# Performance work log

Measured on AMD Instinct MI355X. Metric: run time of the kernel, lower is better.

## Reference

```python
import jax, jax.numpy as jnp
import numpy as np

TEMPERATURE = 0.1


def setup_inputs() -> dict:
    key = jax.random.key(0)
    ks = jax.random.split(key, 8)
    B = 16384
    yonehot = jax.random.uniform(ks[0], (B, 10), dtype=jnp.float32)
    # MLP params (10 -> 128 -> 512 -> 784); uniform-positive so proba > 0 strictly
    W1 = jax.random.uniform(ks[1], (10, 128), dtype=jnp.float32) * 0.05
    b1 = jax.random.uniform(ks[2], (128,), dtype=jnp.float32) * 0.01
    W2 = jax.random.uniform(ks[3], (128, 512), dtype=jnp.float32) * 0.05
    b2 = jax.random.uniform(ks[4], (512,), dtype=jnp.float32) * 0.01
    W3 = jax.random.uniform(ks[5], (512, 784), dtype=jnp.float32) * 0.05
    b3 = jax.random.uniform(ks[6], (784,), dtype=jnp.float32) * 0.01
    return {"yonehot": yonehot, "W1": W1, "b1": b1, "W2": W2, "b2": b2,
            "W3": W3, "b3": b3, "k": 128}


def _mlp(yonehot, W1, b1, W2, b2, W3, b3):
    h = jax.nn.relu(yonehot @ W1 + b1)
    h = jax.nn.relu(h @ W2 + b2)
    return jax.nn.relu(h @ W3 + b3)  # (B, 784) probability map


def _reparametrize(proba, k, rng):
    # k-step Gumbel-softmax sampling, accumulated: img = sum_i softmax((log p + g_i)/T)
    logp = jnp.log(proba)
    keys = jax.random.split(rng, k)

    def step(acc, kk):
        u = jax.random.uniform(kk, proba.shape, dtype=proba.dtype)
        gumbel = -jnp.log(-jnp.log(u))
        acc = acc + jax.nn.softmax((logp + gumbel) / TEMPERATURE, axis=-1)
        return acc, None

    img, _ = jax.lax.scan(step, jnp.zeros_like(proba), keys)
    return img


def reference(yonehot, W1, b1, W2, b2, W3, b3, k):
    proba = _mlp(yonehot, W1, b1, W2, b2, W3, b3)
    img = _reparametrize(proba, k, jax.random.key(1))
    return img, proba
```

## Files before the change

kernel.cpp:

```cpp
#include <hip/hip_runtime.h>
#include <stdint.h>

#define LN2F 0.69314718055994530942f

__device__ __forceinline__ uint32_t rotl32(uint32_t x, int r){ return (x<<r)|(x>>(32-r)); }

__device__ __forceinline__ void tf2x32(uint32_t ks0, uint32_t ks1, uint32_t ks2,
                                       uint32_t x0, uint32_t x1,
                                       uint32_t &o0, uint32_t &o1){
  x0 += ks0; x1 += ks1;
#define TF_R4(a,b,c,d) \
  x0+=x1; x1=rotl32(x1,a); x1^=x0; \
  x0+=x1; x1=rotl32(x1,b); x1^=x0; \
  x0+=x1; x1=rotl32(x1,c); x1^=x0; \
  x0+=x1; x1=rotl32(x1,d); x1^=x0;
  TF_R4(13,15,26,6);  x0+=ks1; x1+=ks2+1u;
  TF_R4(17,29,16,24); x0+=ks2; x1+=ks0+2u;
  TF_R4(13,15,26,6);  x0+=ks0; x1+=ks1+3u;
  TF_R4(17,29,16,24); x0+=ks1; x1+=ks2+4u;
  TF_R4(13,15,26,6);  x0+=ks2; x1+=ks0+5u;
#undef TF_R4
  o0=x0; o1=x1;
}

__global__ __launch_bounds__(256) void mlp1_kernel(
    const float* __restrict__ y, const float* __restrict__ W1,
    const float* __restrict__ b1, float* __restrict__ h1){
  int idx = blockIdx.x*256 + threadIdx.x;
  int r = idx >> 7, c = idx & 127;
  float acc = b1[c];
#pragma unroll
  for (int k=0;k<10;k++) acc = fmaf(y[r*10+k], W1[k*128+c], acc);
  h1[idx] = fmaxf(acc, 0.f);
}

__global__ __launch_bounds__(256) void gemm_relu_kernel(
    const float* __restrict__ A, const float* __restrict__ B,
    const float* __restrict__ bias, float* __restrict__ C,
    int N, int K){
  __shared__ float As[64][33];
  __shared__ float Bs[32][64];
  const int tid = threadIdx.x;
  const int tx = tid & 15, ty = tid >> 4;
  const int r0 = blockIdx.y*64, c0 = blockIdx.x*64;
  float acc[4][4] = {};
  for (int k0=0; k0<K; k0+=32){
#pragma unroll
    for (int i=0;i<8;i++){
      int flat = tid + i*256;
      int ar = flat>>5, ac = flat&31;
      As[ar][ac] = A[(size_t)(r0+ar)*K + (k0+ac)];
    }
#pragma unroll
    for (int i=0;i<8;i++){
      int flat = tid + i*256;
      int br = flat>>6, bc = flat&63;
      int gc = c0+bc;
      Bs[br][bc] = (gc<N) ? B[(size_t)(k0+br)*N + gc] : 0.f;
    }
    __syncthreads();
#pragma unroll
    for (int kk=0;kk<32;kk++){
      float a0=As[ty*4+0][kk], a1=As[ty*4+1][kk], a2=As[ty*4+2][kk], a3=As[ty*4+3][kk];
      float4 b = *(const float4*)&Bs[kk][tx*4];
      acc[0][0]=fmaf(a0,b.x,acc[0][0]); acc[0][1]=fmaf(a0,b.y,acc[0][1]);
      acc[0][2]=fmaf(a0,b.z,acc[0][2]); acc[0][3]=fmaf(a0,b.w,acc[0][3]);
      acc[1][0]=fmaf(a1,b.x,acc[1][0]); acc[1][1]=fmaf(a1,b.y,acc[1][1]);
      acc[1][2]=fmaf(a1,b.z,acc[1][2]); acc[1][3]=fmaf(a1,b.w,acc[1][3]);
      acc[2][0]=fmaf(a2,b.x,acc[2][0]); acc[2][1]=fmaf(a2,b.y,acc[2][1]);
      acc[2][2]=fmaf(a2,b.z,acc[2][2]); acc[2][3]=fmaf(a2,b.w,acc[2][3]);
      acc[3][0]=fmaf(a3,b.x,acc[3][0]); acc[3][1]=fmaf(a3,b.y,acc[3][1]);
      acc[3][2]=fmaf(a3,b.z,acc[3][2]); acc[3][3]=fmaf(a3,b.w,acc[3][3]);
    }
    __syncthreads();
  }
#pragma unroll
  for (int i=0;i<4;i++){
    int r = r0 + ty*4 + i;
#pragma unroll
    for (int j=0;j<4;j++){
      int c = c0 + tx*4 + j;
      if (c < N) C[(size_t)r*N + c] = fmaxf(acc[i][j] + bias[c], 0.f);
    }
  }
}

__global__ __launch_bounds__(256) void reparam_kernel(
    const float* __restrict__ proba, float* __restrict__ img){
  __shared__ uint32_t skeys[256];
  const int tid = threadIdx.x;
  if (tid < 128){
    uint32_t y0,y1;
    tf2x32(0u, 1u, 0x1BD11BDBu, 0u, (uint32_t)tid, y0, y1);
    skeys[2*tid] = y0; skeys[2*tid+1] = y1;
  }
  __syncthreads();

  const int lane = tid & 63;
  const int wv   = tid >> 6;
  const int row  = blockIdx.x*4 + wv;
  const float* pr = proba + (size_t)row*784;

  float lp[13], acc[13];
#pragma unroll
  for (int m=0;m<13;m++){
    int c = lane + 64*m;
    bool v = (m<12) || (lane<16);
    float a = v ? pr[c] : 1.f;
    lp[m] = 10.f*__builtin_amdgcn_logf(a);
    acc[m] = 0.f;
  }

  const uint32_t ebase = (uint32_t)row*784u + (uint32_t)lane;

  for (int s=0;s<128;s++){
    uint32_t k0 = skeys[2*s], k1 = skeys[2*s+1];
    uint32_t k2 = k0 ^ k1 ^ 0x1BD11BDAu;
    float zb[13];
    float mx = -INFINITY;
#pragma unroll
    for (int m=0;m<13;m++){
      uint32_t o0,o1;
      tf2x32(k0,k1,k2, 0u, ebase + 64u*(uint32_t)m, o0,o1);
      uint32_t bits = o0 ^ o1;
      float u = __uint_as_float((bits>>9) | 0x3F800000u) - 1.f;
      float t = u - 1.f;
      float P = fmaf(t, 1.f/7.f, -1.f/6.f);
      P = fmaf(t, P, 1.f/5.f);
      P = fmaf(t, P, -1.f/4.f);
      P = fmaf(t, P, 1.f/3.f);
      P = fmaf(t, P, -1.f/2.f);
      P = fmaf(t, P, 1.f);
      float w_poly = -t*P;
      float w_hw = -LN2F*__builtin_amdgcn_logf(u);
      float w = (u > 0.875f) ? w_poly : w_hw;
      float z = fmaf(-10.f, __builtin_amdgcn_logf(w), lp[m]);
      if (m==12 && lane>=16) z = -INFINITY;
      zb[m]=z;
      mx = fmaxf(mx,z);
    }
#pragma unroll
    for (int off=1; off<64; off<<=1)
      mx = fmaxf(mx, __shfl_xor(mx, off, 64));
    float ssum=0.f;
#pragma unroll
    for (int m=0;m<13;m++){
      float e2 = __builtin_amdgcn_exp2f(zb[m]-mx);
      zb[m]=e2; ssum+=e2;
    }
#pragma unroll
    for (int off=1; off<64; off<<=1)
      ssum += __shfl_xor(ssum, off, 64);
    float rs = __builtin_amdgcn_rcpf(ssum);
#pragma unroll
    for (int m=0;m<13;m++) acc[m] = fmaf(zb[m], rs, acc[m]);
  }

  float* op = img + (size_t)row*784;
#pragma unroll
  for (int m=0;m<13;m++){
    int c = lane + 64*m;
    if (m<12 || lane<16) op[c]=acc[m];
  }
}

extern "C" void kernel_launch(void* const* d_in, const int* in_sizes, int n_in,
                              void* d_out, int out_size, void* d_ws, size_t ws_size,
                              hipStream_t stream){
  const float* y  = (const float*)d_in[0];
  const float* W1 = (const float*)d_in[1];
  const float* b1 = (const float*)d_in[2];
  const float* W2 = (const float*)d_in[3];
  const float* b2 = (const float*)d_in[4];
  const float* W3 = (const float*)d_in[5];
  const float* b3 = (const float*)d_in[6];

  float* img   = (float*)d_out;
  float* proba = (float*)d_out + (size_t)16384*784;

  float* h1 = img;
  float* h2 = img + (size_t)16384*128;

  mlp1_kernel<<<8192, 256, 0, stream>>>(y, W1, b1, h1);
  gemm_relu_kernel<<<dim3(8, 256), 256, 0, stream>>>(h1, W2, b2, h2, 512, 128);
  gemm_relu_kernel<<<dim3(13, 256), 256, 0, stream>>>(h2, W3, b3, proba, 784, 512);
  reparam_kernel<<<4096, 256, 0, stream>>>(proba, img);
}
```

Measured before the change: 3.964 ms.

## Replace log/exp softmax with tenth-power ratio form and use alignbit rotates

Measured after the change: 4.027 ms. About the same (+1.6%).

```diff
diff --git a/kernel.cpp b/kernel.cpp
--- a/kernel.cpp
+++ b/kernel.cpp
@@ -3,17 +3,17 @@
 
 #define LN2F 0.69314718055994530942f
 
-__device__ __forceinline__ uint32_t rotl32(uint32_t x, int r){ return (x<<r)|(x>>(32-r)); }
+#define ROTL(x,r) __builtin_amdgcn_alignbit((x), (x), 32-(r))
 
 __device__ __forceinline__ void tf2x32(uint32_t ks0, uint32_t ks1, uint32_t ks2,
                                        uint32_t x0, uint32_t x1,
                                        uint32_t &o0, uint32_t &o1){
   x0 += ks0; x1 += ks1;
 #define TF_R4(a,b,c,d) \
-  x0+=x1; x1=rotl32(x1,a); x1^=x0; \
-  x0+=x1; x1=rotl32(x1,b); x1^=x0; \
-  x0+=x1; x1=rotl32(x1,c); x1^=x0; \
-  x0+=x1; x1=rotl32(x1,d); x1^=x0;
+  x0+=x1; x1=ROTL(x1,a); x1^=x0; \
+  x0+=x1; x1=ROTL(x1,b); x1^=x0; \
+  x0+=x1; x1=ROTL(x1,c); x1^=x0; \
+  x0+=x1; x1=ROTL(x1,d); x1^=x0;
   TF_R4(13,15,26,6);  x0+=ks1; x1+=ks2+1u;
   TF_R4(17,29,16,24); x0+=ks2; x1+=ks0+2u;
   TF_R4(13,15,26,6);  x0+=ks0; x1+=ks1+3u;
@@ -85,7 +85,7 @@
   }
 }
 
-__global__ __launch_bounds__(256) void reparam_kernel(
+__global__ __launch_bounds__(256, 4) void reparam_kernel(
     const float* __restrict__ proba, float* __restrict__ img){
   __shared__ uint32_t skeys[256];
   const int tid = threadIdx.x;
@@ -101,13 +101,11 @@
   const int row  = blockIdx.x*4 + wv;
   const float* pr = proba + (size_t)row*784;
 
-  float lp[13], acc[13];
+  float p[13], acc[13];
 #pragma unroll
   for (int m=0;m<13;m++){
     int c = lane + 64*m;
-    bool v = (m<12) || (lane<16);
-    float a = v ? pr[c] : 1.f;
-    lp[m] = 10.f*__builtin_amdgcn_logf(a);
+    p[m] = ((m<12) || (lane<16)) ? pr[c] : 0.f;
     acc[m] = 0.f;
   }
 
@@ -116,44 +114,50 @@
   for (int s=0;s<128;s++){
     uint32_t k0 = skeys[2*s], k1 = skeys[2*s+1];
     uint32_t k2 = k0 ^ k1 ^ 0x1BD11BDAu;
-    float zb[13];
-    float mx = -INFINITY;
+    float v[13];
+    float mx = 0.f;
 #pragma unroll
     for (int m=0;m<13;m++){
       uint32_t o0,o1;
       tf2x32(k0,k1,k2, 0u, ebase + 64u*(uint32_t)m, o0,o1);
       uint32_t bits = o0 ^ o1;
-      float u = __uint_as_float((bits>>9) | 0x3F800000u) - 1.f;
-      float t = u - 1.f;
+      float f = __uint_as_float((bits>>9) | 0x3F800000u);
+      float u = f - 1.f;
+      float t = f - 2.f;
       float P = fmaf(t, 1.f/7.f, -1.f/6.f);
       P = fmaf(t, P, 1.f/5.f);
       P = fmaf(t, P, -1.f/4.f);
       P = fmaf(t, P, 1.f/3.f);
       P = fmaf(t, P, -1.f/2.f);
       P = fmaf(t, P, 1.f);
-      float w_poly = -t*P;
+      float w_poly = (2.f - f) * P;
       float w_hw = -LN2F*__builtin_amdgcn_logf(u);
       float w = (u > 0.875f) ? w_poly : w_hw;
-      float z = fmaf(-10.f, __builtin_amdgcn_logf(w), lp[m]);
-      if (m==12 && lane>=16) z = -INFINITY;
-      zb[m]=z;
-      mx = fmaxf(mx,z);
+      float vm = p[m] * __builtin_amdgcn_rcpf(w);
+      v[m] = vm;
+      mx = fmaxf(mx, vm);
     }
 #pragma unroll
     for (int off=1; off<64; off<<=1)
       mx = fmaxf(mx, __shfl_xor(mx, off, 64));
-    float ssum=0.f;
+    float rmx = __builtin_amdgcn_rcpf(mx);
+    float ssum = 0.f;
 #pragma unroll
     for (int m=0;m<13;m++){
-      float e2 = __builtin_amdgcn_exp2f(zb[m]-mx);
-      zb[m]=e2; ssum+=e2;
+      float r  = v[m]*rmx;
+      float r2 = r*r;
+      float r4 = r2*r2;
+      float r8 = r4*r4;
+      float e  = r8*r2;
+      v[m] = e;
+      ssum += e;
     }
 #pragma unroll
     for (int off=1; off<64; off<<=1)
       ssum += __shfl_xor(ssum, off, 64);
     float rs = __builtin_amdgcn_rcpf(ssum);
 #pragma unroll
-    for (int m=0;m<13;m++) acc[m] = fmaf(zb[m], rs, acc[m]);
+    for (int m=0;m<13;m++) acc[m] = fmaf(v[m], rs, acc[m]);
   }
 
   float* op = img + (size_t)row*784;
```
